# Optimization experiments

Measured on AMD Instinct MI355X. Metric: run time of the kernel, lower is better.

Reference implementation:

```python
import jax, jax.numpy as jnp
import numpy as np

VOCAB = 32000
D_MODEL = 1024


def setup_inputs() -> dict:
    key = jax.random.key(0)
    k = jax.random.split(key, 8)
    B, H, T, S = 8, 16, 128, 512
    src = jax.random.randint(k[0], (B, S), 0, VOCAB)
    decode_output = jax.random.normal(k[1], (B, T, D_MODEL), dtype=jnp.float32)
    decode_attn = jax.random.uniform(k[2], (B, H, T, S), dtype=jnp.float32)
    memory = jax.random.normal(k[3], (B, S, D_MODEL), dtype=jnp.float32)
    W_gen = jax.random.normal(k[4], (VOCAB, D_MODEL), dtype=jnp.float32) * (1.0 / np.sqrt(D_MODEL))
    b_gen = jnp.zeros((VOCAB,), dtype=jnp.float32)
    W_prob = jax.random.normal(k[5], (1, 2 * D_MODEL), dtype=jnp.float32) * (1.0 / np.sqrt(2 * D_MODEL))
    b_prob = jnp.zeros((1,), dtype=jnp.float32)
    return {"src": src, "decode_output": decode_output, "decode_attn": decode_attn,
            "memory": memory, "W_gen": W_gen, "b_gen": b_gen,
            "W_prob": W_prob, "b_prob": b_prob}


def reference(src, decode_output, decode_attn, memory, W_gen, b_gen, W_prob, b_prob):
    # mean over heads: [B, T, S]
    attn = jnp.mean(decode_attn, axis=1)
    B, T, S = attn.shape
    V = W_gen.shape[0]

    # generation logits: [B, T, V]
    gen_logits = jnp.einsum('btd,vd->btv', decode_output, W_gen) + b_gen

    # context vector: [B, T, D]
    context = jnp.einsum('bts,bsd->btd', attn, memory)

    # scatter-add copy distribution over vocab: [B, T, V]
    src_exp = jnp.broadcast_to(src[:, None, :], (B, T, S))  # token ids per step
    b_idx = jnp.arange(B)[:, None, None]
    t_idx = jnp.arange(T)[None, :, None]
    copy_logits = jnp.zeros((B, T, V), dtype=attn.dtype).at[b_idx, t_idx, src_exp].add(attn)

    # copy gate: sigmoid(Linear([context; decode_output])) -> [B, T, 1]
    cat = jnp.concatenate([context, decode_output], axis=-1)
    prob = jax.nn.sigmoid(jnp.einsum('btd,od->bto', cat, W_prob) + b_prob)

    gen_p = prob * jax.nn.softmax(gen_logits, axis=-1)
    copy_p = (1.0 - prob) * jax.nn.softmax(copy_logits, axis=-1)
    final = gen_p + copy_p
    return jnp.log(final).reshape(-1, V)
```

## Files before the change

### kernel.cpp

```cpp
#include <hip/hip_runtime.h>
#include <hip/hip_bf16.h>
#include <cstddef>
#include <cstdint>

#define BB 8
#define HH 16
#define TT 128
#define SS 512
#define DD 1024
#define VV 32000
#define MM (BB * TT)

typedef float f32x4 __attribute__((ext_vector_type(4)));
typedef short short8v __attribute__((ext_vector_type(8)));
typedef unsigned short ushort8v __attribute__((ext_vector_type(8)));

__device__ __forceinline__ unsigned short f2bf(float x) {
    __hip_bfloat16 h = __float2bfloat16(x);
    return __builtin_bit_cast(unsigned short, h);
}

__device__ __forceinline__ float wave_sum(float v) {
#pragma unroll
    for (int o = 1; o < 64; o <<= 1) v += __shfl_xor(v, o);
    return v;
}
__device__ __forceinline__ float wave_max(float v) {
#pragma unroll
    for (int o = 1; o < 64; o <<= 1) v = fmaxf(v, __shfl_xor(v, o));
    return v;
}
__device__ __forceinline__ float block_sum(float v, float* red, int tid) {
    v = wave_sum(v);
    __syncthreads();
    if ((tid & 63) == 0) red[tid >> 6] = v;
    __syncthreads();
    return red[0] + red[1] + red[2] + red[3];
}
__device__ __forceinline__ float block_max(float v, float* red, int tid) {
    v = wave_max(v);
    __syncthreads();
    if ((tid & 63) == 0) red[tid >> 6] = v;
    __syncthreads();
    return fmaxf(fmaxf(red[0], red[1]), fmaxf(red[2], red[3]));
}

__global__ void k_pm_init(int* pos_map, float* zg) {
    int i = blockIdx.x * 256 + threadIdx.x;
    if (i < BB * VV) pos_map[i] = 0x7fffffff;
    if (i < MM) zg[i] = 0.0f;
}

__global__ void k_pm_build(const int* __restrict__ src, int* pos_map) {
    int b = blockIdx.x, s = threadIdx.x;
    int tok = src[b * SS + s];
    atomicMin(&pos_map[b * VV + tok], s);
}

__global__ __launch_bounds__(256) void k_cast(const float* __restrict__ in,
                                              unsigned short* __restrict__ outp, int n8) {
    int stride = gridDim.x * 256;
    for (int i = blockIdx.x * 256 + threadIdx.x; i < n8; i += stride) {
        const float4* p = reinterpret_cast<const float4*>(in + (size_t)i * 8);
        float4 a = p[0], b = p[1];
        ushort8v u;
        u[0] = f2bf(a.x); u[1] = f2bf(a.y); u[2] = f2bf(a.z); u[3] = f2bf(a.w);
        u[4] = f2bf(b.x); u[5] = f2bf(b.y); u[6] = f2bf(b.z); u[7] = f2bf(b.w);
        *reinterpret_cast<ushort8v*>(outp + (size_t)i * 8) = u;
    }
}

__global__ __launch_bounds__(256) void k_vecdots(const float* __restrict__ memory,
                                                 const float* __restrict__ dec,
                                                 const float* __restrict__ wprob,
                                                 float* mw, float* dw) {
    int row = blockIdx.x * 4 + (threadIdx.x >> 6);
    int lane = threadIdx.x & 63;
    const float4* srcv;
    const float4* wv;
    if (row < BB * SS) {
        srcv = reinterpret_cast<const float4*>(memory + (size_t)row * DD);
        wv = reinterpret_cast<const float4*>(wprob);
    } else {
        srcv = reinterpret_cast<const float4*>(dec + (size_t)(row - BB * SS) * DD);
        wv = reinterpret_cast<const float4*>(wprob + DD);
    }
    float sum = 0.f;
#pragma unroll
    for (int k = 0; k < 4; ++k) {
        int idx = lane + 64 * k;
        float4 a = srcv[idx];
        float4 w = wv[idx];
        sum += a.x * w.x + a.y * w.y + a.z * w.z + a.w * w.w;
    }
    sum = wave_sum(sum);
    if (lane == 0) {
        if (row < BB * SS) mw[row] = sum;
        else dw[row - BB * SS] = sum;
    }
}

__global__ __launch_bounds__(256) void k_row(const float* __restrict__ dattn,
                                             const int* __restrict__ src,
                                             const int* __restrict__ pos_map,
                                             const float* __restrict__ mw,
                                             const float* __restrict__ dw,
                                             const float* __restrict__ bprob,
                                             float* __restrict__ e_vals,
                                             float* __restrict__ prob,
                                             float* __restrict__ zc,
                                             float* __restrict__ c0) {
    int bt = blockIdx.x;
    int b = bt >> 7;
    int t = bt & 127;
    int tid = threadIdx.x;
    __shared__ float a_row[SS];
    __shared__ float vals[SS];
    __shared__ float red[4];

    for (int s = tid; s < SS; s += 256) {
        const float* base = dattn + ((size_t)b * HH * TT + t) * SS + s;
        float sum = 0.f;
#pragma unroll
        for (int h = 0; h < HH; ++h) sum += base[(size_t)h * TT * SS];
        a_row[s] = sum * 0.0625f;
        vals[s] = 0.f;
    }
    __syncthreads();
    for (int s = tid; s < SS; s += 256) {
        int rep = pos_map[b * VV + src[b * SS + s]];
        atomicAdd(&vals[rep], a_row[s]);
    }
    __syncthreads();
    float psum = 0.f;
    for (int s = tid; s < SS; s += 256) psum += a_row[s] * mw[b * SS + s];
    psum = block_sum(psum, red, tid);
    float z = psum + dw[bt] + bprob[0];
    float p = 1.0f / (1.0f + __expf(-z));
    float mxv = -3.4e38f;
    for (int s = tid; s < SS; s += 256) {
        int rep = pos_map[b * VV + src[b * SS + s]];
        if (rep == s) mxv = fmaxf(mxv, vals[s]);
    }
    mxv = block_max(mxv, red, tid);
    float m_c = fmaxf(0.0f, mxv);
    float sexp = 0.f, cnt = 0.f;
    for (int s = tid; s < SS; s += 256) {
        int rep = pos_map[b * VV + src[b * SS + s]];
        float e = 0.0f;
        if (rep == s) {
            e = __expf(vals[s] - m_c);
            sexp += e;
            cnt += 1.0f;
        }
        e_vals[(size_t)bt * SS + s] = e;
    }
    sexp = block_sum(sexp, red, tid);
    cnt = block_sum(cnt, red, tid);
    if (tid == 0) {
        prob[bt] = p;
        zc[bt] = ((float)VV - cnt) * __expf(-m_c) + sexp;
        c0[bt] = __expf(-m_c);
    }
}

#define Bk 64
#define NKT 16

__global__ __launch_bounds__(512, 2) void k_gemm_bf(const unsigned short* __restrict__ Abf,
                                                    const unsigned short* __restrict__ Wbf,
                                                    const float* __restrict__ bgen,
                                                    float* __restrict__ out,
                                                    float* __restrict__ zg) {
    __shared__ unsigned short lds[65536];

    int tid = threadIdx.x;
    int p = blockIdx.x;
    int xcd = p & 7, jj = p >> 3;
    int wg = (xcd < 4 ? xcd * 63 : 252 + (xcd - 4) * 62) + jj;
    int mt = wg & 3, nt = wg >> 2;
    int m0 = mt * 256, v0 = nt * 256;

    int lane = tid & 63, w = tid >> 6;
    int wm = w & 1, wn = w >> 1;

    int rsub = lane >> 3;
    int csw = (lane & 7) ^ rsub;
    const unsigned short* gA = Abf + (size_t)(m0 + w * 8 + rsub) * DD + csw * 8;
    const unsigned short* gB = Wbf + (size_t)(v0 + w * 8 + rsub) * DD + csw * 8;
    int lds_w = w * 512;

#define STAGE(sl, t) do {                                                              \
    unsigned short* As_ = lds + (sl) * 32768;                                          \
    unsigned short* Bs_ = lds + 16384 + (sl) * 32768;                                  \
    int k0_ = (t) * Bk;                                                                \
    _Pragma("unroll")                                                                  \
    for (int q = 0; q < 4; ++q)                                                        \
        __builtin_amdgcn_global_load_lds(                                              \
            (const __attribute__((address_space(1))) void*)(gA + (size_t)(q * 64) * DD + k0_), \
            (__attribute__((address_space(3))) void*)(As_ + q * 4096 + lds_w), 16, 0, 0); \
    _Pragma("unroll")                                                                  \
    for (int q = 0; q < 4; ++q)                                                        \
        __builtin_amdgcn_global_load_lds(                                              \
            (const __attribute__((address_space(1))) void*)(gB + (size_t)(q * 64) * DD + k0_), \
            (__attribute__((address_space(3))) void*)(Bs_ + q * 4096 + lds_w), 16, 0, 0); \
} while (0)

    int lr = lane & 15, kg = lane >> 4, l7 = lane & 7;

    f32x4 acc[8][4] = {};

    STAGE(0, 0);
    STAGE(1, 1);
    asm volatile("s_waitcnt vmcnt(8)" ::: "memory");
    __builtin_amdgcn_s_barrier();

#pragma unroll 2
    for (int t = 0; t < NKT; ++t) {
        int sl = t & 1;
        unsigned short* As_ = lds + sl * 32768;
        unsigned short* Bs_ = lds + 16384 + sl * 32768;

        short8v af[2][8], bfr[2][4];
#pragma unroll
        for (int ks = 0; ks < 2; ++ks) {
            int chunk = ((ks * 4 + kg) ^ l7) * 8;
#pragma unroll
            for (int i = 0; i < 8; ++i)
                af[ks][i] = *reinterpret_cast<const short8v*>(
                    &As_[(wm * 128 + i * 16 + lr) * 64 + chunk]);
#pragma unroll
            for (int j = 0; j < 4; ++j)
                bfr[ks][j] = *reinterpret_cast<const short8v*>(
                    &Bs_[(wn * 64 + j * 16 + lr) * 64 + chunk]);
        }
        asm volatile("s_waitcnt lgkmcnt(0)" ::: "memory");
        __builtin_amdgcn_s_barrier();

        if (t + 2 < NKT) STAGE(sl, t + 2);

        __builtin_amdgcn_s_setprio(1);
#pragma unroll
        for (int i = 0; i < 8; ++i)
#pragma unroll
            for (int j = 0; j < 4; ++j) {
                acc[i][j] = __builtin_amdgcn_mfma_f32_16x16x32_bf16(af[0][i], bfr[0][j], acc[i][j], 0, 0, 0);
                acc[i][j] = __builtin_amdgcn_mfma_f32_16x16x32_bf16(af[1][i], bfr[1][j], acc[i][j], 0, 0, 0);
            }
        __builtin_amdgcn_s_setprio(0);

        if (t + 1 < NKT) {
            if (t + 2 < NKT)
                asm volatile("s_waitcnt vmcnt(8)" ::: "memory");
            else
                asm volatile("s_waitcnt vmcnt(0)" ::: "memory");
            __builtin_amdgcn_s_barrier();
        }
    }
#undef STAGE

    int colb = lane & 15, rgrp = lane >> 4;
#pragma unroll
    for (int i = 0; i < 8; ++i) {
        float es0 = 0.f, es1 = 0.f, es2 = 0.f, es3 = 0.f;
        int gmb = m0 + wm * 128 + i * 16 + rgrp * 4;
#pragma unroll
        for (int j = 0; j < 4; ++j) {
            int gv = v0 + wn * 64 + j * 16 + colb;
            float bgj = bgen[gv];
            float v0f = acc[i][j][0] + bgj;
            float v1f = acc[i][j][1] + bgj;
            float v2f = acc[i][j][2] + bgj;
            float v3f = acc[i][j][3] + bgj;
            out[(size_t)(gmb + 0) * VV + gv] = v0f;
            out[(size_t)(gmb + 1) * VV + gv] = v1f;
            out[(size_t)(gmb + 2) * VV + gv] = v2f;
            out[(size_t)(gmb + 3) * VV + gv] = v3f;
            es0 += __expf(v0f); es1 += __expf(v1f);
            es2 += __expf(v2f); es3 += __expf(v3f);
        }
        float es[4] = {es0, es1, es2, es3};
#pragma unroll
        for (int rr = 0; rr < 4; ++rr) {
            float e = es[rr];
            e += __shfl_xor(e, 1); e += __shfl_xor(e, 2);
            e += __shfl_xor(e, 4); e += __shfl_xor(e, 8);
            if (colb == 0) atomicAdd(&zg[gmb + rr], e);
        }
    }
}

#define FBb 128
#define FLDK 40

__global__ __launch_bounds__(256) void k_gemm_f32(const float* __restrict__ A,
                                                  const float* __restrict__ Wg,
                                                  const float* __restrict__ bgen,
                                                  float* __restrict__ out,
                                                  float* __restrict__ zg) {
    __shared__ unsigned short As[FBb * FLDK];
    __shared__ unsigned short Bs[FBb * FLDK];
    int tid = threadIdx.x;
    int bid = blockIdx.x;
    int mt = bid & 7;
    int nt = bid >> 3;
    int m0 = mt * FBb, v0 = nt * FBb;
    int lane = tid & 63, wid = tid >> 6;
    int wr = (wid >> 1) * 64, wc = (wid & 1) * 64;
    int lr = lane & 15, lk = (lane >> 4) << 3;
    int r = tid >> 1, c0 = (tid & 1) << 4;

    f32x4 acc[4][4] = {};

    for (int k0 = 0; k0 < DD; k0 += 32) {
        {
            const float4* pa = reinterpret_cast<const float4*>(A + (size_t)(m0 + r) * DD + k0 + c0);
            float4 x0 = pa[0], x1 = pa[1], x2 = pa[2], x3 = pa[3];
            ushort8v u0, u1;
            u0[0] = f2bf(x0.x); u0[1] = f2bf(x0.y); u0[2] = f2bf(x0.z); u0[3] = f2bf(x0.w);
            u0[4] = f2bf(x1.x); u0[5] = f2bf(x1.y); u0[6] = f2bf(x1.z); u0[7] = f2bf(x1.w);
            u1[0] = f2bf(x2.x); u1[1] = f2bf(x2.y); u1[2] = f2bf(x2.z); u1[3] = f2bf(x2.w);
            u1[4] = f2bf(x3.x); u1[5] = f2bf(x3.y); u1[6] = f2bf(x3.z); u1[7] = f2bf(x3.w);
            *reinterpret_cast<ushort8v*>(&As[r * FLDK + c0]) = u0;
            *reinterpret_cast<ushort8v*>(&As[r * FLDK + c0 + 8]) = u1;

            const float4* pb = reinterpret_cast<const float4*>(Wg + (size_t)(v0 + r) * DD + k0 + c0);
            float4 y0 = pb[0], y1 = pb[1], y2 = pb[2], y3 = pb[3];
            ushort8v w0, w1;
            w0[0] = f2bf(y0.x); w0[1] = f2bf(y0.y); w0[2] = f2bf(y0.z); w0[3] = f2bf(y0.w);
            w0[4] = f2bf(y1.x); w0[5] = f2bf(y1.y); w0[6] = f2bf(y1.z); w0[7] = f2bf(y1.w);
            w1[0] = f2bf(y2.x); w1[1] = f2bf(y2.y); w1[2] = f2bf(y2.z); w1[3] = f2bf(y2.w);
            w1[4] = f2bf(y3.x); w1[5] = f2bf(y3.y); w1[6] = f2bf(y3.z); w1[7] = f2bf(y3.w);
            *reinterpret_cast<ushort8v*>(&Bs[r * FLDK + c0]) = w0;
            *reinterpret_cast<ushort8v*>(&Bs[r * FLDK + c0 + 8]) = w1;
        }
        __syncthreads();

        short8v af[4], bfr[4];
#pragma unroll
        for (int i = 0; i < 4; ++i)
            af[i] = *reinterpret_cast<const short8v*>(&As[(wr + i * 16 + lr) * FLDK + lk]);
#pragma unroll
        for (int j = 0; j < 4; ++j)
            bfr[j] = *reinterpret_cast<const short8v*>(&Bs[(wc + j * 16 + lr) * FLDK + lk]);
#pragma unroll
        for (int i = 0; i < 4; ++i)
#pragma unroll
            for (int j = 0; j < 4; ++j)
                acc[i][j] = __builtin_amdgcn_mfma_f32_16x16x32_bf16(af[i], bfr[j], acc[i][j], 0, 0, 0);
        __syncthreads();
    }

    int colb = lane & 15;
    int rgrp = lane >> 4;
#pragma unroll
    for (int i = 0; i < 4; ++i) {
        float es0 = 0.f, es1 = 0.f, es2 = 0.f, es3 = 0.f;
        int gmb = m0 + wr + i * 16 + rgrp * 4;
#pragma unroll
        for (int j = 0; j < 4; ++j) {
            int gv = v0 + wc + j * 16 + colb;
            float bgj = bgen[gv];
            float v0f = acc[i][j][0] + bgj;
            float v1f = acc[i][j][1] + bgj;
            float v2f = acc[i][j][2] + bgj;
            float v3f = acc[i][j][3] + bgj;
            out[(size_t)(gmb + 0) * VV + gv] = v0f;
            out[(size_t)(gmb + 1) * VV + gv] = v1f;
            out[(size_t)(gmb + 2) * VV + gv] = v2f;
            out[(size_t)(gmb + 3) * VV + gv] = v3f;
            es0 += __expf(v0f); es1 += __expf(v1f);
            es2 += __expf(v2f); es3 += __expf(v3f);
        }
        float es[4] = {es0, es1, es2, es3};
#pragma unroll
        for (int rr = 0; rr < 4; ++rr) {
            float e = es[rr];
            e += __shfl_xor(e, 1); e += __shfl_xor(e, 2);
            e += __shfl_xor(e, 4); e += __shfl_xor(e, 8);
            if (colb == 0) atomicAdd(&zg[gmb + rr], e);
        }
    }
}

__global__ __launch_bounds__(256) void k_final(float* __restrict__ gen,
                                               const int* __restrict__ pos_map,
                                               const float* __restrict__ e_vals,
                                               const float* __restrict__ prob,
                                               const float* __restrict__ zc,
                                               const float* __restrict__ c0,
                                               const float* __restrict__ zg) {
    int m = blockIdx.x;
    int b = m >> 7;
    int tid = threadIdx.x;
    float p = prob[m];
    float A1 = p / zg[m];
    float A2 = (1.0f - p) / zc[m];
    float cc = c0[m];
    const float* ev = e_vals + (size_t)m * SS;
    float4* row = reinterpret_cast<float4*>(gen + (size_t)m * VV);
    const int4* pm = reinterpret_cast<const int4*>(pos_map + b * VV);
    for (int i = tid; i < VV / 4; i += 256) {
        float4 g = row[i];
        int4 rp = pm[i];
        float4 o;
        o.x = __logf(A1 * __expf(g.x) + A2 * ((rp.x < SS) ? ev[rp.x] : cc));
        o.y = __logf(A1 * __expf(g.y) + A2 * ((rp.y < SS) ? ev[rp.y] : cc));
        o.z = __logf(A1 * __expf(g.z) + A2 * ((rp.z < SS) ? ev[rp.z] : cc));
        o.w = __logf(A1 * __expf(g.w) + A2 * ((rp.w < SS) ? ev[rp.w] : cc));
        row[i] = o;
    }
}

extern "C" void kernel_launch(void* const* d_in, const int* in_sizes, int n_in,
                              void* d_out, int out_size, void* d_ws, size_t ws_size,
                              hipStream_t stream) {
    const int* src = (const int*)d_in[0];
    const float* dec = (const float*)d_in[1];
    const float* dattn = (const float*)d_in[2];
    const float* mem = (const float*)d_in[3];
    const float* wgen = (const float*)d_in[4];
    const float* bgen = (const float*)d_in[5];
    const float* wprob = (const float*)d_in[6];
    const float* bprob = (const float*)d_in[7];
    float* out = (float*)d_out;
    char* ws = (char*)d_ws;

    int* pos_map = (int*)(ws + 0);
    float* e_vals = (float*)(ws + 1048576);
    float* mw   = (float*)(ws + 3145728);
    float* dw   = (float*)(ws + 3145728 + 16384);
    float* prob = (float*)(ws + 3145728 + 20480);
    float* zc   = (float*)(ws + 3145728 + 24576);
    float* c0   = (float*)(ws + 3145728 + 28672);
    float* zg   = (float*)(ws + 3145728 + 32768);
    unsigned short* Wbf = (unsigned short*)(ws + 3211264);
    unsigned short* Abf = (unsigned short*)(ws + 3211264 + 65536000);
    const size_t NEEDED = 3211264ull + 65536000ull + 2097152ull;

    k_pm_init<<<(BB * VV + 255) / 256, 256, 0, stream>>>(pos_map, zg);
    k_pm_build<<<BB, SS, 0, stream>>>(src, pos_map);
    k_vecdots<<<(BB * SS + MM) / 4, 256, 0, stream>>>(mem, dec, wprob, mw, dw);
    k_row<<<MM, 256, 0, stream>>>(dattn, src, pos_map, mw, dw, bprob, e_vals, prob, zc, c0);

    if (ws_size >= NEEDED) {
        k_cast<<<2048, 256, 0, stream>>>(wgen, Wbf, VV * DD / 8);
        k_cast<<<512, 256, 0, stream>>>(dec, Abf, MM * DD / 8);
        k_gemm_bf<<<(MM / 256) * (VV / 256), 512, 0, stream>>>(Abf, Wbf, bgen, out, zg);
    } else {
        k_gemm_f32<<<(MM / FBb) * (VV / FBb), 256, 0, stream>>>(dec, wgen, bgen, out, zg);
    }
    k_final<<<MM, 256, 0, stream>>>(out, pos_map, e_vals, prob, zc, c0, zg);
}
```

Before: 249.7 us.

## Split GEMM k-loop into finer MFMA phases and store exp logits as bf16

The bf16 GEMM main loop is restructured into four sub-phases per K tile. LDS fragment reads, staged A/B global-to-LDS loads and MFMA blocks are interleaved with barriers and sched_barrier, and fewer fragments are held in registers at once. The epilogue can now write exp(logits) as bf16 into an extra workspace buffer instead of fp32 logits. The final kernel then reads that half-size buffer and skips the exp, cutting memory traffic between the two kernels. This costs extra workspace and bf16 rounding of the generation probabilities, and the added barriers may stall the pipeline.

```diff
diff --git a/kernel.cpp b/kernel.cpp
--- a/kernel.cpp
+++ b/kernel.cpp
@@ -18,6 +18,10 @@
 __device__ __forceinline__ unsigned short f2bf(float x) {
     __hip_bfloat16 h = __float2bfloat16(x);
     return __builtin_bit_cast(unsigned short, h);
+}
+__device__ __forceinline__ float bf2f(unsigned short u) {
+    unsigned int x = ((unsigned int)u) << 16;
+    return __builtin_bit_cast(float, x);
 }
 
 __device__ __forceinline__ float wave_sum(float v) {
@@ -167,10 +171,12 @@
 #define Bk 64
 #define NKT 16
 
+template <int EPI>
 __global__ __launch_bounds__(512, 2) void k_gemm_bf(const unsigned short* __restrict__ Abf,
                                                     const unsigned short* __restrict__ Wbf,
                                                     const float* __restrict__ bgen,
                                                     float* __restrict__ out,
+                                                    unsigned short* __restrict__ ebuf,
                                                     float* __restrict__ zg) {
     __shared__ unsigned short lds[65536];
 
@@ -190,74 +196,127 @@
     const unsigned short* gB = Wbf + (size_t)(v0 + w * 8 + rsub) * DD + csw * 8;
     int lds_w = w * 512;
 
-#define STAGE(sl, t) do {                                                              \
-    unsigned short* As_ = lds + (sl) * 32768;                                          \
-    unsigned short* Bs_ = lds + 16384 + (sl) * 32768;                                  \
-    int k0_ = (t) * Bk;                                                                \
-    _Pragma("unroll")                                                                  \
-    for (int q = 0; q < 4; ++q)                                                        \
-        __builtin_amdgcn_global_load_lds(                                              \
-            (const __attribute__((address_space(1))) void*)(gA + (size_t)(q * 64) * DD + k0_), \
-            (__attribute__((address_space(3))) void*)(As_ + q * 4096 + lds_w), 16, 0, 0); \
-    _Pragma("unroll")                                                                  \
-    for (int q = 0; q < 4; ++q)                                                        \
-        __builtin_amdgcn_global_load_lds(                                              \
-            (const __attribute__((address_space(1))) void*)(gB + (size_t)(q * 64) * DD + k0_), \
-            (__attribute__((address_space(3))) void*)(Bs_ + q * 4096 + lds_w), 16, 0, 0); \
-} while (0)
+#define STAGE_A(SL, T, Q)                                                                     \
+    __builtin_amdgcn_global_load_lds(                                                         \
+        (const __attribute__((address_space(1))) void*)(gA + (size_t)((Q) * 64) * DD + (T) * Bk), \
+        (__attribute__((address_space(3))) void*)(lds + (SL) * 32768 + (Q) * 4096 + lds_w), 16, 0, 0)
+#define STAGE_B(SL, T, Q)                                                                     \
+    __builtin_amdgcn_global_load_lds(                                                         \
+        (const __attribute__((address_space(1))) void*)(gB + (size_t)((Q) * 64) * DD + (T) * Bk), \
+        (__attribute__((address_space(3))) void*)(lds + 16384 + (SL) * 32768 + (Q) * 4096 + lds_w), 16, 0, 0)
 
     int lr = lane & 15, kg = lane >> 4, l7 = lane & 7;
 
     f32x4 acc[8][4] = {};
 
-    STAGE(0, 0);
-    STAGE(1, 1);
+#pragma unroll
+    for (int q = 0; q < 4; ++q) STAGE_B(0, 0, q);
+#pragma unroll
+    for (int q = 0; q < 4; ++q) STAGE_A(0, 0, q);
+#pragma unroll
+    for (int q = 0; q < 4; ++q) STAGE_B(1, 1, q);
+#pragma unroll
+    for (int q = 0; q < 4; ++q) STAGE_A(1, 1, q);
     asm volatile("s_waitcnt vmcnt(8)" ::: "memory");
     __builtin_amdgcn_s_barrier();
 
 #pragma unroll 2
     for (int t = 0; t < NKT; ++t) {
-        int sl = t & 1;
+        const int sl = t & 1;
         unsigned short* As_ = lds + sl * 32768;
         unsigned short* Bs_ = lds + 16384 + sl * 32768;
-
-        short8v af[2][8], bfr[2][4];
-#pragma unroll
-        for (int ks = 0; ks < 2; ++ks) {
-            int chunk = ((ks * 4 + kg) ^ l7) * 8;
-#pragma unroll
-            for (int i = 0; i < 8; ++i)
-                af[ks][i] = *reinterpret_cast<const short8v*>(
-                    &As_[(wm * 128 + i * 16 + lr) * 64 + chunk]);
+        short8v af[4], bfr[4];
+        const bool stA = (t >= 1) && (t + 1 < NKT);
+
+        {
+            const int chunk = (kg ^ l7) * 8;
 #pragma unroll
             for (int j = 0; j < 4; ++j)
-                bfr[ks][j] = *reinterpret_cast<const short8v*>(
-                    &Bs_[(wn * 64 + j * 16 + lr) * 64 + chunk]);
-        }
-        asm volatile("s_waitcnt lgkmcnt(0)" ::: "memory");
-        __builtin_amdgcn_s_barrier();
-
-        if (t + 2 < NKT) STAGE(sl, t + 2);
-
-        __builtin_amdgcn_s_setprio(1);
-#pragma unroll
-        for (int i = 0; i < 8; ++i)
-#pragma unroll
-            for (int j = 0; j < 4; ++j) {
-                acc[i][j] = __builtin_amdgcn_mfma_f32_16x16x32_bf16(af[0][i], bfr[0][j], acc[i][j], 0, 0, 0);
-                acc[i][j] = __builtin_amdgcn_mfma_f32_16x16x32_bf16(af[1][i], bfr[1][j], acc[i][j], 0, 0, 0);
+                bfr[j] = *reinterpret_cast<const short8v*>(&Bs_[(wn * 64 + j * 16 + lr) * 64 + chunk]);
+#pragma unroll
+            for (int i = 0; i < 4; ++i)
+                af[i] = *reinterpret_cast<const short8v*>(&As_[(wm * 128 + i * 16 + lr) * 64 + chunk]);
+            if (stA) { STAGE_A(sl ^ 1, t + 1, 0); STAGE_A(sl ^ 1, t + 1, 2); }
+            __builtin_amdgcn_s_barrier();
+            asm volatile("s_waitcnt lgkmcnt(0)" ::: "memory");
+            __builtin_amdgcn_sched_barrier(0);
+            __builtin_amdgcn_s_setprio(1);
+#pragma unroll
+            for (int i = 0; i < 4; ++i)
+#pragma unroll
+                for (int j = 0; j < 4; ++j)
+                    acc[i][j] = __builtin_amdgcn_mfma_f32_16x16x32_bf16(af[i], bfr[j], acc[i][j], 0, 0, 0);
+            __builtin_amdgcn_s_setprio(0);
+            __builtin_amdgcn_s_barrier();
+        }
+        {
+            const int chunk = (kg ^ l7) * 8;
+#pragma unroll
+            for (int i = 0; i < 4; ++i)
+                af[i] = *reinterpret_cast<const short8v*>(&As_[(wm * 128 + (i + 4) * 16 + lr) * 64 + chunk]);
+            if (stA) { STAGE_A(sl ^ 1, t + 1, 1); STAGE_A(sl ^ 1, t + 1, 3); }
+            __builtin_amdgcn_s_barrier();
+            asm volatile("s_waitcnt lgkmcnt(0)" ::: "memory");
+            __builtin_amdgcn_sched_barrier(0);
+            __builtin_amdgcn_s_setprio(1);
+#pragma unroll
+            for (int i = 0; i < 4; ++i)
+#pragma unroll
+                for (int j = 0; j < 4; ++j)
+                    acc[i + 4][j] = __builtin_amdgcn_mfma_f32_16x16x32_bf16(af[i], bfr[j], acc[i + 4][j], 0, 0, 0);
+            __builtin_amdgcn_s_setprio(0);
+            __builtin_amdgcn_s_barrier();
+        }
+        {
+            const int chunk = ((4 + kg) ^ l7) * 8;
+#pragma unroll
+            for (int j = 0; j < 4; ++j)
+                bfr[j] = *reinterpret_cast<const short8v*>(&Bs_[(wn * 64 + j * 16 + lr) * 64 + chunk]);
+#pragma unroll
+            for (int i = 0; i < 4; ++i)
+                af[i] = *reinterpret_cast<const short8v*>(&As_[(wm * 128 + i * 16 + lr) * 64 + chunk]);
+            __builtin_amdgcn_s_barrier();
+            asm volatile("s_waitcnt lgkmcnt(0)" ::: "memory");
+            __builtin_amdgcn_sched_barrier(0);
+            __builtin_amdgcn_s_setprio(1);
+#pragma unroll
+            for (int i = 0; i < 4; ++i)
+#pragma unroll
+                for (int j = 0; j < 4; ++j)
+                    acc[i][j] = __builtin_amdgcn_mfma_f32_16x16x32_bf16(af[i], bfr[j], acc[i][j], 0, 0, 0);
+            __builtin_amdgcn_s_setprio(0);
+            __builtin_amdgcn_s_barrier();
+        }
+        {
+            const int chunk = ((4 + kg) ^ l7) * 8;
+#pragma unroll
+            for (int i = 0; i < 4; ++i)
+                af[i] = *reinterpret_cast<const short8v*>(&As_[(wm * 128 + (i + 4) * 16 + lr) * 64 + chunk]);
+            if (t + 2 < NKT) {
+                STAGE_B(sl, t + 2, 0); STAGE_B(sl, t + 2, 1);
+                STAGE_B(sl, t + 2, 2); STAGE_B(sl, t + 2, 3);
             }
-        __builtin_amdgcn_s_setprio(0);
-
-        if (t + 1 < NKT) {
-            if (t + 2 < NKT)
-                asm volatile("s_waitcnt vmcnt(8)" ::: "memory");
-            else
-                asm volatile("s_waitcnt vmcnt(0)" ::: "memory");
-            __builtin_amdgcn_s_barrier();
-        }
-    }
-#undef STAGE
+            __builtin_amdgcn_s_barrier();
+            asm volatile("s_waitcnt lgkmcnt(0)" ::: "memory");
+            __builtin_amdgcn_sched_barrier(0);
+            __builtin_amdgcn_s_setprio(1);
+#pragma unroll
+            for (int i = 0; i < 4; ++i)
+#pragma unroll
+                for (int j = 0; j < 4; ++j)
+                    acc[i + 4][j] = __builtin_amdgcn_mfma_f32_16x16x32_bf16(af[i], bfr[j], acc[i + 4][j], 0, 0, 0);
+            __builtin_amdgcn_s_setprio(0);
+            if (t + 1 < NKT) {
+                if (t + 2 < NKT)
+                    asm volatile("s_waitcnt vmcnt(4)" ::: "memory");
+                else
+                    asm volatile("s_waitcnt vmcnt(0)" ::: "memory");
+                __builtin_amdgcn_s_barrier();
+            }
+        }
+    }
+#undef STAGE_A
+#undef STAGE_B
 
     int colb = lane & 15, rgrp = lane >> 4;
 #pragma unroll
@@ -272,12 +331,19 @@
             float v1f = acc[i][j][1] + bgj;
             float v2f = acc[i][j][2] + bgj;
             float v3f = acc[i][j][3] + bgj;
-            out[(size_t)(gmb + 0) * VV + gv] = v0f;
-            out[(size_t)(gmb + 1) * VV + gv] = v1f;
-            out[(size_t)(gmb + 2) * VV + gv] = v2f;
-            out[(size_t)(gmb + 3) * VV + gv] = v3f;
-            es0 += __expf(v0f); es1 += __expf(v1f);
-            es2 += __expf(v2f); es3 += __expf(v3f);
+            float e0 = __expf(v0f), e1 = __expf(v1f), e2 = __expf(v2f), e3 = __expf(v3f);
+            if constexpr (EPI == 1) {
+                ebuf[(size_t)(gmb + 0) * VV + gv] = f2bf(e0);
+                ebuf[(size_t)(gmb + 1) * VV + gv] = f2bf(e1);
+                ebuf[(size_t)(gmb + 2) * VV + gv] = f2bf(e2);
+                ebuf[(size_t)(gmb + 3) * VV + gv] = f2bf(e3);
+            } else {
+                out[(size_t)(gmb + 0) * VV + gv] = v0f;
+                out[(size_t)(gmb + 1) * VV + gv] = v1f;
+                out[(size_t)(gmb + 2) * VV + gv] = v2f;
+                out[(size_t)(gmb + 3) * VV + gv] = v3f;
+            }
+            es0 += e0; es1 += e1; es2 += e2; es3 += e3;
         }
         float es[4] = {es0, es1, es2, es3};
 #pragma unroll
@@ -383,7 +449,9 @@
     }
 }
 
+template <int RD16>
 __global__ __launch_bounds__(256) void k_final(float* __restrict__ gen,
+                                               const unsigned short* __restrict__ ebuf,
                                                const int* __restrict__ pos_map,
                                                const float* __restrict__ e_vals,
                                                const float* __restrict__ prob,
@@ -400,15 +468,29 @@
     const float* ev = e_vals + (size_t)m * SS;
     float4* row = reinterpret_cast<float4*>(gen + (size_t)m * VV);
     const int4* pm = reinterpret_cast<const int4*>(pos_map + b * VV);
-    for (int i = tid; i < VV / 4; i += 256) {
-        float4 g = row[i];
-        int4 rp = pm[i];
-        float4 o;
-        o.x = __logf(A1 * __expf(g.x) + A2 * ((rp.x < SS) ? ev[rp.x] : cc));
-        o.y = __logf(A1 * __expf(g.y) + A2 * ((rp.y < SS) ? ev[rp.y] : cc));
-        o.z = __logf(A1 * __expf(g.z) + A2 * ((rp.z < SS) ? ev[rp.z] : cc));
-        o.w = __logf(A1 * __expf(g.w) + A2 * ((rp.w < SS) ? ev[rp.w] : cc));
-        row[i] = o;
+    if constexpr (RD16 == 1) {
+        const ushort4* erow = reinterpret_cast<const ushort4*>(ebuf + (size_t)m * VV);
+        for (int i = tid; i < VV / 4; i += 256) {
+            ushort4 ee = erow[i];
+            int4 rp = pm[i];
+            float4 o;
+            o.x = __logf(A1 * bf2f(ee.x) + A2 * ((rp.x < SS) ? ev[rp.x] : cc));
+            o.y = __logf(A1 * bf2f(ee.y) + A2 * ((rp.y < SS) ? ev[rp.y] : cc));
+            o.z = __logf(A1 * bf2f(ee.z) + A2 * ((rp.z < SS) ? ev[rp.z] : cc));
+            o.w = __logf(A1 * bf2f(ee.w) + A2 * ((rp.w < SS) ? ev[rp.w] : cc));
+            row[i] = o;
+        }
+    } else {
+        for (int i = tid; i < VV / 4; i += 256) {
+            float4 g = row[i];
+            int4 rp = pm[i];
+            float4 o;
+            o.x = __logf(A1 * __expf(g.x) + A2 * ((rp.x < SS) ? ev[rp.x] : cc));
+            o.y = __logf(A1 * __expf(g.y) + A2 * ((rp.y < SS) ? ev[rp.y] : cc));
+            o.z = __logf(A1 * __expf(g.z) + A2 * ((rp.z < SS) ? ev[rp.z] : cc));
+            o.w = __logf(A1 * __expf(g.w) + A2 * ((rp.w < SS) ? ev[rp.w] : cc));
+            row[i] = o;
+        }
     }
 }
 
@@ -436,7 +518,9 @@
     float* zg   = (float*)(ws + 3145728 + 32768);
     unsigned short* Wbf = (unsigned short*)(ws + 3211264);
     unsigned short* Abf = (unsigned short*)(ws + 3211264 + 65536000);
-    const size_t NEEDED = 3211264ull + 65536000ull + 2097152ull;
+    unsigned short* Ebf = (unsigned short*)(ws + 3211264 + 65536000 + 2097152);
+    const size_t NEEDED  = 3211264ull + 65536000ull + 2097152ull;
+    const size_t NEEDED2 = NEEDED + 65536000ull;
 
     k_pm_init<<<(BB * VV + 255) / 256, 256, 0, stream>>>(pos_map, zg);
     k_pm_build<<<BB, SS, 0, stream>>>(src, pos_map);
@@ -446,9 +530,15 @@
     if (ws_size >= NEEDED) {
         k_cast<<<2048, 256, 0, stream>>>(wgen, Wbf, VV * DD / 8);
         k_cast<<<512, 256, 0, stream>>>(dec, Abf, MM * DD / 8);
-        k_gemm_bf<<<(MM / 256) * (VV / 256), 512, 0, stream>>>(Abf, Wbf, bgen, out, zg);
+        if (ws_size >= NEEDED2) {
+            k_gemm_bf<1><<<(MM / 256) * (VV / 256), 512, 0, stream>>>(Abf, Wbf, bgen, out, Ebf, zg);
+            k_final<1><<<MM, 256, 0, stream>>>(out, Ebf, pos_map, e_vals, prob, zc, c0, zg);
+        } else {
+            k_gemm_bf<0><<<(MM / 256) * (VV / 256), 512, 0, stream>>>(Abf, Wbf, bgen, out, Ebf, zg);
+            k_final<0><<<MM, 256, 0, stream>>>(out, Ebf, pos_map, e_vals, prob, zc, c0, zg);
+        }
     } else {
         k_gemm_f32<<<(MM / FBb) * (VV / FBb), 256, 0, stream>>>(dec, wgen, bgen, out, zg);
-    }
-    k_final<<<MM, 256, 0, stream>>>(out, pos_map, e_vals, prob, zc, c0, zg);
-}
+        k_final<0><<<MM, 256, 0, stream>>>(out, Ebf, pos_map, e_vals, prob, zc, c0, zg);
+    }
+}
```

New measurement: 246.7 us. Within noise of the previous version (-1.2%).

## Shrink GEMM tiles, single-buffer LDS, and pass bf16 exp values to final kernel

Applied to the files above, without the earlier changes.

The bf16 GEMM tile shrinks from 256x256 to 128x256 with a single LDS buffer, and launch bounds allow 4 blocks per CU, which raises occupancy and the number of workgroups. When workspace allows, the GEMM epilogue writes exp(logit) as bf16 into a separate buffer instead of fp32 logits. The final kernel then reads half the bytes and skips the exp. This trades fp32 logit precision for bf16 exp values, adds a 64MB workspace requirement, and drops double buffering, so load latency is hidden only by occupancy.

```diff
diff --git a/kernel.cpp b/kernel.cpp
--- a/kernel.cpp
+++ b/kernel.cpp
@@ -18,6 +18,10 @@
 __device__ __forceinline__ unsigned short f2bf(float x) {
     __hip_bfloat16 h = __float2bfloat16(x);
     return __builtin_bit_cast(unsigned short, h);
+}
+__device__ __forceinline__ float bf2f(unsigned short u) {
+    unsigned int x = ((unsigned int)u) << 16;
+    return __builtin_bit_cast(float, x);
 }
 
 __device__ __forceinline__ float wave_sum(float v) {
@@ -167,103 +171,106 @@
 #define Bk 64
 #define NKT 16
 
-__global__ __launch_bounds__(512, 2) void k_gemm_bf(const unsigned short* __restrict__ Abf,
+#define AS1 __attribute__((address_space(1)))
+#define AS3 __attribute__((address_space(3)))
+
+template <int EPI>
+__global__ __launch_bounds__(512, 4) void k_gemm_bf(const unsigned short* __restrict__ Abf,
                                                     const unsigned short* __restrict__ Wbf,
                                                     const float* __restrict__ bgen,
                                                     float* __restrict__ out,
+                                                    unsigned short* __restrict__ ebuf,
                                                     float* __restrict__ zg) {
-    __shared__ unsigned short lds[65536];
+    __shared__ unsigned short lds[24576];
 
     int tid = threadIdx.x;
     int p = blockIdx.x;
-    int xcd = p & 7, jj = p >> 3;
-    int wg = (xcd < 4 ? xcd * 63 : 252 + (xcd - 4) * 62) + jj;
-    int mt = wg & 3, nt = wg >> 2;
-    int m0 = mt * 256, v0 = nt * 256;
+    int wg = (p & 7) * 125 + (p >> 3);
+    int mt = wg & 7, nt = wg >> 3;
+    int m0 = mt * 128, v0 = nt * 256;
 
     int lane = tid & 63, w = tid >> 6;
     int wm = w & 1, wn = w >> 1;
 
-    int rsub = lane >> 3;
-    int csw = (lane & 7) ^ rsub;
-    const unsigned short* gA = Abf + (size_t)(m0 + w * 8 + rsub) * DD + csw * 8;
-    const unsigned short* gB = Wbf + (size_t)(v0 + w * 8 + rsub) * DD + csw * 8;
-    int lds_w = w * 512;
-
-#define STAGE(sl, t) do {                                                              \
-    unsigned short* As_ = lds + (sl) * 32768;                                          \
-    unsigned short* Bs_ = lds + 16384 + (sl) * 32768;                                  \
-    int k0_ = (t) * Bk;                                                                \
+    int srow = tid >> 3;
+    int schunk = (tid & 7) ^ (srow & 7);
+    const unsigned short* gA = Abf + (size_t)(m0 + srow) * DD + schunk * 8;
+    const unsigned short* gB = Wbf + (size_t)(v0 + srow) * DD + schunk * 8;
+
+#define STAGE(T) do {                                                                  \
+    size_t ko_ = (size_t)(T) * Bk;                                                     \
+    _Pragma("unroll")                                                                  \
+    for (int q = 0; q < 2; ++q)                                                        \
+        __builtin_amdgcn_global_load_lds(                                              \
+            (const AS1 void*)(gA + (size_t)q * 64 * DD + ko_),                         \
+            (AS3 void*)(lds + q * 4096 + tid * 8), 16, 0, 0);                          \
     _Pragma("unroll")                                                                  \
     for (int q = 0; q < 4; ++q)                                                        \
         __builtin_amdgcn_global_load_lds(                                              \
-            (const __attribute__((address_space(1))) void*)(gA + (size_t)(q * 64) * DD + k0_), \
-            (__attribute__((address_space(3))) void*)(As_ + q * 4096 + lds_w), 16, 0, 0); \
-    _Pragma("unroll")                                                                  \
-    for (int q = 0; q < 4; ++q)                                                        \
-        __builtin_amdgcn_global_load_lds(                                              \
-            (const __attribute__((address_space(1))) void*)(gB + (size_t)(q * 64) * DD + k0_), \
-            (__attribute__((address_space(3))) void*)(Bs_ + q * 4096 + lds_w), 16, 0, 0); \
+            (const AS1 void*)(gB + (size_t)q * 64 * DD + ko_),                         \
+            (AS3 void*)(lds + 8192 + q * 4096 + tid * 8), 16, 0, 0);                   \
 } while (0)
 
-    int lr = lane & 15, kg = lane >> 4, l7 = lane & 7;
-
-    f32x4 acc[8][4] = {};
-
-    STAGE(0, 0);
-    STAGE(1, 1);
-    asm volatile("s_waitcnt vmcnt(8)" ::: "memory");
+    int lr = lane & 15, kg = lane >> 4, l7s = (lane & 15) & 7;
+
+    f32x4 acc[4][4] = {};
+
+    STAGE(0);
+    asm volatile("s_waitcnt vmcnt(0)" ::: "memory");
     __builtin_amdgcn_s_barrier();
 
-#pragma unroll 2
     for (int t = 0; t < NKT; ++t) {
-        int sl = t & 1;
-        unsigned short* As_ = lds + sl * 32768;
-        unsigned short* Bs_ = lds + 16384 + sl * 32768;
-
-        short8v af[2][8], bfr[2][4];
-#pragma unroll
-        for (int ks = 0; ks < 2; ++ks) {
-            int chunk = ((ks * 4 + kg) ^ l7) * 8;
-#pragma unroll
-            for (int i = 0; i < 8; ++i)
-                af[ks][i] = *reinterpret_cast<const short8v*>(
-                    &As_[(wm * 128 + i * 16 + lr) * 64 + chunk]);
+        short8v af[4], bfr[4];
+        {
+            const int c = (kg ^ l7s) * 8;
+#pragma unroll
+            for (int i = 0; i < 4; ++i)
+                af[i] = *reinterpret_cast<const short8v*>(&lds[(wm * 64 + i * 16 + lr) * 64 + c]);
 #pragma unroll
             for (int j = 0; j < 4; ++j)
-                bfr[ks][j] = *reinterpret_cast<const short8v*>(
-                    &Bs_[(wn * 64 + j * 16 + lr) * 64 + chunk]);
-        }
-        asm volatile("s_waitcnt lgkmcnt(0)" ::: "memory");
-        __builtin_amdgcn_s_barrier();
-
-        if (t + 2 < NKT) STAGE(sl, t + 2);
-
-        __builtin_amdgcn_s_setprio(1);
-#pragma unroll
-        for (int i = 0; i < 8; ++i)
-#pragma unroll
-            for (int j = 0; j < 4; ++j) {
-                acc[i][j] = __builtin_amdgcn_mfma_f32_16x16x32_bf16(af[0][i], bfr[0][j], acc[i][j], 0, 0, 0);
-                acc[i][j] = __builtin_amdgcn_mfma_f32_16x16x32_bf16(af[1][i], bfr[1][j], acc[i][j], 0, 0, 0);
+                bfr[j] = *reinterpret_cast<const short8v*>(&lds[8192 + (wn * 64 + j * 16 + lr) * 64 + c]);
+            asm volatile("s_waitcnt lgkmcnt(0)" ::: "memory");
+            __builtin_amdgcn_sched_barrier(0);
+            __builtin_amdgcn_s_setprio(1);
+#pragma unroll
+            for (int i = 0; i < 4; ++i)
+#pragma unroll
+                for (int j = 0; j < 4; ++j)
+                    acc[i][j] = __builtin_amdgcn_mfma_f32_16x16x32_bf16(af[i], bfr[j], acc[i][j], 0, 0, 0);
+            __builtin_amdgcn_s_setprio(0);
+        }
+        {
+            const int c = ((4 + kg) ^ l7s) * 8;
+#pragma unroll
+            for (int i = 0; i < 4; ++i)
+                af[i] = *reinterpret_cast<const short8v*>(&lds[(wm * 64 + i * 16 + lr) * 64 + c]);
+#pragma unroll
+            for (int j = 0; j < 4; ++j)
+                bfr[j] = *reinterpret_cast<const short8v*>(&lds[8192 + (wn * 64 + j * 16 + lr) * 64 + c]);
+            asm volatile("s_waitcnt lgkmcnt(0)" ::: "memory");
+            __builtin_amdgcn_sched_barrier(0);
+            __builtin_amdgcn_s_barrier();
+            if (t + 1 < NKT) STAGE(t + 1);
+            __builtin_amdgcn_s_setprio(1);
+#pragma unroll
+            for (int i = 0; i < 4; ++i)
+#pragma unroll
+                for (int j = 0; j < 4; ++j)
+                    acc[i][j] = __builtin_amdgcn_mfma_f32_16x16x32_bf16(af[i], bfr[j], acc[i][j], 0, 0, 0);
+            __builtin_amdgcn_s_setprio(0);
+            if (t + 1 < NKT) {
+                asm volatile("s_waitcnt vmcnt(0)" ::: "memory");
+                __builtin_amdgcn_s_barrier();
             }
-        __builtin_amdgcn_s_setprio(0);
-
-        if (t + 1 < NKT) {
-            if (t + 2 < NKT)
-                asm volatile("s_waitcnt vmcnt(8)" ::: "memory");
-            else
-                asm volatile("s_waitcnt vmcnt(0)" ::: "memory");
-            __builtin_amdgcn_s_barrier();
         }
     }
 #undef STAGE
 
     int colb = lane & 15, rgrp = lane >> 4;
 #pragma unroll
-    for (int i = 0; i < 8; ++i) {
+    for (int i = 0; i < 4; ++i) {
         float es0 = 0.f, es1 = 0.f, es2 = 0.f, es3 = 0.f;
-        int gmb = m0 + wm * 128 + i * 16 + rgrp * 4;
+        int gmb = m0 + wm * 64 + i * 16 + rgrp * 4;
 #pragma unroll
         for (int j = 0; j < 4; ++j) {
             int gv = v0 + wn * 64 + j * 16 + colb;
@@ -272,12 +279,19 @@
             float v1f = acc[i][j][1] + bgj;
             float v2f = acc[i][j][2] + bgj;
             float v3f = acc[i][j][3] + bgj;
-            out[(size_t)(gmb + 0) * VV + gv] = v0f;
-            out[(size_t)(gmb + 1) * VV + gv] = v1f;
-            out[(size_t)(gmb + 2) * VV + gv] = v2f;
-            out[(size_t)(gmb + 3) * VV + gv] = v3f;
-            es0 += __expf(v0f); es1 += __expf(v1f);
-            es2 += __expf(v2f); es3 += __expf(v3f);
+            float e0 = __expf(v0f), e1 = __expf(v1f), e2 = __expf(v2f), e3 = __expf(v3f);
+            if constexpr (EPI == 1) {
+                ebuf[(size_t)(gmb + 0) * VV + gv] = f2bf(e0);
+                ebuf[(size_t)(gmb + 1) * VV + gv] = f2bf(e1);
+                ebuf[(size_t)(gmb + 2) * VV + gv] = f2bf(e2);
+                ebuf[(size_t)(gmb + 3) * VV + gv] = f2bf(e3);
+            } else {
+                out[(size_t)(gmb + 0) * VV + gv] = v0f;
+                out[(size_t)(gmb + 1) * VV + gv] = v1f;
+                out[(size_t)(gmb + 2) * VV + gv] = v2f;
+                out[(size_t)(gmb + 3) * VV + gv] = v3f;
+            }
+            es0 += e0; es1 += e1; es2 += e2; es3 += e3;
         }
         float es[4] = {es0, es1, es2, es3};
 #pragma unroll
@@ -383,7 +397,9 @@
     }
 }
 
+template <int RD16>
 __global__ __launch_bounds__(256) void k_final(float* __restrict__ gen,
+                                               const unsigned short* __restrict__ ebuf,
                                                const int* __restrict__ pos_map,
                                                const float* __restrict__ e_vals,
                                                const float* __restrict__ prob,
@@ -400,15 +416,34 @@
     const float* ev = e_vals + (size_t)m * SS;
     float4* row = reinterpret_cast<float4*>(gen + (size_t)m * VV);
     const int4* pm = reinterpret_cast<const int4*>(pos_map + b * VV);
-    for (int i = tid; i < VV / 4; i += 256) {
-        float4 g = row[i];
-        int4 rp = pm[i];
-        float4 o;
-        o.x = __logf(A1 * __expf(g.x) + A2 * ((rp.x < SS) ? ev[rp.x] : cc));
-        o.y = __logf(A1 * __expf(g.y) + A2 * ((rp.y < SS) ? ev[rp.y] : cc));
-        o.z = __logf(A1 * __expf(g.z) + A2 * ((rp.z < SS) ? ev[rp.z] : cc));
-        o.w = __logf(A1 * __expf(g.w) + A2 * ((rp.w < SS) ? ev[rp.w] : cc));
-        row[i] = o;
+    if constexpr (RD16 == 1) {
+        const ushort8v* erow = reinterpret_cast<const ushort8v*>(ebuf + (size_t)m * VV);
+        for (int i = tid; i < VV / 8; i += 256) {
+            ushort8v ee = erow[i];
+            int4 rp0 = pm[2 * i], rp1 = pm[2 * i + 1];
+            float4 o0, o1;
+            o0.x = __logf(A1 * bf2f(ee[0]) + A2 * ((rp0.x < SS) ? ev[rp0.x] : cc));
+            o0.y = __logf(A1 * bf2f(ee[1]) + A2 * ((rp0.y < SS) ? ev[rp0.y] : cc));
+            o0.z = __logf(A1 * bf2f(ee[2]) + A2 * ((rp0.z < SS) ? ev[rp0.z] : cc));
+            o0.w = __logf(A1 * bf2f(ee[3]) + A2 * ((rp0.w < SS) ? ev[rp0.w] : cc));
+            o1.x = __logf(A1 * bf2f(ee[4]) + A2 * ((rp1.x < SS) ? ev[rp1.x] : cc));
+            o1.y = __logf(A1 * bf2f(ee[5]) + A2 * ((rp1.y < SS) ? ev[rp1.y] : cc));
+            o1.z = __logf(A1 * bf2f(ee[6]) + A2 * ((rp1.z < SS) ? ev[rp1.z] : cc));
+            o1.w = __logf(A1 * bf2f(ee[7]) + A2 * ((rp1.w < SS) ? ev[rp1.w] : cc));
+            row[2 * i] = o0;
+            row[2 * i + 1] = o1;
+        }
+    } else {
+        for (int i = tid; i < VV / 4; i += 256) {
+            float4 g = row[i];
+            int4 rp = pm[i];
+            float4 o;
+            o.x = __logf(A1 * __expf(g.x) + A2 * ((rp.x < SS) ? ev[rp.x] : cc));
+            o.y = __logf(A1 * __expf(g.y) + A2 * ((rp.y < SS) ? ev[rp.y] : cc));
+            o.z = __logf(A1 * __expf(g.z) + A2 * ((rp.z < SS) ? ev[rp.z] : cc));
+            o.w = __logf(A1 * __expf(g.w) + A2 * ((rp.w < SS) ? ev[rp.w] : cc));
+            row[i] = o;
+        }
     }
 }
 
@@ -436,7 +471,9 @@
     float* zg   = (float*)(ws + 3145728 + 32768);
     unsigned short* Wbf = (unsigned short*)(ws + 3211264);
     unsigned short* Abf = (unsigned short*)(ws + 3211264 + 65536000);
-    const size_t NEEDED = 3211264ull + 65536000ull + 2097152ull;
+    unsigned short* Ebf = (unsigned short*)(ws + 3211264 + 65536000 + 2097152);
+    const size_t NEEDED  = 3211264ull + 65536000ull + 2097152ull;
+    const size_t NEEDED2 = NEEDED + 65536000ull;
 
     k_pm_init<<<(BB * VV + 255) / 256, 256, 0, stream>>>(pos_map, zg);
     k_pm_build<<<BB, SS, 0, stream>>>(src, pos_map);
@@ -446,9 +483,15 @@
     if (ws_size >= NEEDED) {
         k_cast<<<2048, 256, 0, stream>>>(wgen, Wbf, VV * DD / 8);
         k_cast<<<512, 256, 0, stream>>>(dec, Abf, MM * DD / 8);
-        k_gemm_bf<<<(MM / 256) * (VV / 256), 512, 0, stream>>>(Abf, Wbf, bgen, out, zg);
+        if (ws_size >= NEEDED2) {
+            k_gemm_bf<1><<<(MM / 128) * (VV / 256), 512, 0, stream>>>(Abf, Wbf, bgen, out, Ebf, zg);
+            k_final<1><<<MM, 256, 0, stream>>>(out, Ebf, pos_map, e_vals, prob, zc, c0, zg);
+        } else {
+            k_gemm_bf<0><<<(MM / 128) * (VV / 256), 512, 0, stream>>>(Abf, Wbf, bgen, out, Ebf, zg);
+            k_final<0><<<MM, 256, 0, stream>>>(out, Ebf, pos_map, e_vals, prob, zc, c0, zg);
+        }
     } else {
         k_gemm_f32<<<(MM / FBb) * (VV / FBb), 256, 0, stream>>>(dec, wgen, bgen, out, zg);
-    }
-    k_final<<<MM, 256, 0, stream>>>(out, pos_map, e_vals, prob, zc, c0, zg);
-}
+        k_final<0><<<MM, 256, 0, stream>>>(out, Ebf, pos_map, e_vals, prob, zc, c0, zg);
+    }
+}
```

Result: faster. 230.1 us (-7.9%).
